# Kernel tuning notes

Measured on AMD Instinct MI355X. Metric: run time of the kernel, lower is better.

The kernel has to match this reference:

```python
import jax, jax.numpy as jnp
import numpy as np

D = 2048          # n_embd
F = 1408          # moe_inter_dim
E = 8             # n_routed_experts
TOPK = 2          # n_activated_experts
N_SHARED = 2
ROUTE_SCALE = 1.0


def setup_inputs() -> dict:
    key = jax.random.key(0)
    ks = jax.random.split(key, 8)
    s = 0.02
    x = jax.random.normal(ks[0], (2, 1024, D), dtype=jnp.float32)
    gate_w = jax.random.normal(ks[1], (D, E), dtype=jnp.float32) * s
    Fs = F * N_SHARED
    sw1 = jax.random.normal(ks[2], (D, Fs), dtype=jnp.float32) * s
    sw2 = jax.random.normal(ks[3], (Fs, D), dtype=jnp.float32) * s
    sw3 = jax.random.normal(ks[4], (D, Fs), dtype=jnp.float32) * s
    rw1 = jax.random.normal(ks[5], (E, D, F), dtype=jnp.float32) * s
    rw2 = jax.random.normal(ks[6], (E, F, D), dtype=jnp.float32) * s
    rw3 = jax.random.normal(ks[7], (E, D, F), dtype=jnp.float32) * s
    return {"x": x, "gate_w": gate_w, "sw1": sw1, "sw2": sw2, "sw3": sw3,
            "rw1": rw1, "rw2": rw2, "rw3": rw3}


def _swiglu(x, w1, w2, w3):
    return (jax.nn.silu(x @ w1) * (x @ w3)) @ w2


def reference(x, gate_w, sw1, sw2, sw3, rw1, rw2, rw3):
    B, T, _ = x.shape
    xf = x.reshape(-1, D)                       # [N, D]
    N = xf.shape[0]
    # shared experts (always applied)
    y = _swiglu(xf, sw1, sw2, sw3)              # [N, D]
    # gate: softmax scores, top-k (bias is None since n_embd != 7168; n_groups == 1)
    scores = jax.nn.softmax(xf @ gate_w, axis=-1)       # [N, E]
    weights, indices = jax.lax.top_k(scores, TOPK)       # gathered original scores
    weights = weights * ROUTE_SCALE
    # combine weights per (token, expert); zero for unassigned -> same math as
    # the per-expert gather/scatter loop in the original module
    cw = jnp.zeros((N, E), dtype=xf.dtype).at[jnp.arange(N)[:, None], indices].add(weights)
    for e in range(E):  # fixed small structural loop over experts
        h = _swiglu(xf, rw1[e], rw2[e], rw3[e])  # [N, D]
        y = y + cw[:, e:e + 1] * h
    return y.reshape(B, T, D)
```

## Files before the change

### kernel.cpp

```cpp
#include <hip/hip_runtime.h>
#include <hip/hip_bf16.h>
#include <math.h>

#define D_DIM 2048
#define F_DIM 1408
#define FS_DIM 2816
#define E_NUM 8
#define N_TOK 2048

typedef __attribute__((ext_vector_type(8))) short bf16x8;
typedef __attribute__((ext_vector_type(4))) float f32x4;

__device__ inline short f2bf(float f) {
    __hip_bfloat16 h = __float2bfloat16(f);
    return *reinterpret_cast<short*>(&h);
}
__device__ inline float bf2f(short s) {
    __hip_bfloat16 h; *reinterpret_cast<short*>(&h) = s;
    return __bfloat162float(h);
}
__device__ inline float silu1(float v) { return v / (1.f + expf(-v)); }

__device__ inline void async_copy16(const void* g, void* l) {
    __builtin_amdgcn_global_load_lds(
        (const __attribute__((address_space(1))) void*)g,
        (__attribute__((address_space(3))) void*)l, 16, 0, 0);
}

__device__ inline void t64(const float* in, short* out, int K, int N,
                           int kt, int nt, float (*tile)[65])
{
    int k0 = kt * 64, n0 = nt * 64;
    int t = threadIdx.x, tr = t >> 4, tc4 = (t & 15) * 4;
#pragma unroll
    for (int i = 0; i < 4; ++i) {
        int r = tr + i * 16;
        float4 v = *reinterpret_cast<const float4*>(in + (size_t)(k0 + r) * N + n0 + tc4);
        tile[r][tc4 + 0] = v.x; tile[r][tc4 + 1] = v.y;
        tile[r][tc4 + 2] = v.z; tile[r][tc4 + 3] = v.w;
    }
    __syncthreads();
#pragma unroll
    for (int i = 0; i < 4; ++i) {
        int n = tr + i * 16;
        short4 s4;
        s4.x = f2bf(tile[tc4 + 0][n]);
        s4.y = f2bf(tile[tc4 + 1][n]);
        s4.z = f2bf(tile[tc4 + 2][n]);
        s4.w = f2bf(tile[tc4 + 3][n]);
        *reinterpret_cast<short4*>(out + (size_t)(n0 + n) * K + k0 + tc4) = s4;
    }
}

__global__ __launch_bounds__(256) void prep_kernel(
    const float* __restrict__ x, const float* __restrict__ gw,
    float* __restrict__ assign_w, int* __restrict__ expert_count,
    int* __restrict__ expert_list, short* __restrict__ Xb,
    const float* __restrict__ sw1, short* __restrict__ swt1,
    const float* __restrict__ sw3, short* __restrict__ swt3,
    const float* __restrict__ rw1, short* __restrict__ rwt1,
    const float* __restrict__ rw3, short* __restrict__ rwt3)
{
    __shared__ float tile[64][65];
    int bid = blockIdx.x;
    int tid = threadIdx.x;
    if (bid < 512) {
        int wid = bid * 4 + (tid >> 6);
        int lane = tid & 63;
        const float* xr = x + (size_t)wid * D_DIM;
        float p[E_NUM];
#pragma unroll
        for (int e = 0; e < E_NUM; ++e) p[e] = 0.f;
        for (int d = lane; d < D_DIM; d += 64) {
            float xv = xr[d];
            const float4* g = reinterpret_cast<const float4*>(gw + (size_t)d * E_NUM);
            float4 g0 = g[0], g1 = g[1];
            p[0] = fmaf(xv, g0.x, p[0]); p[1] = fmaf(xv, g0.y, p[1]);
            p[2] = fmaf(xv, g0.z, p[2]); p[3] = fmaf(xv, g0.w, p[3]);
            p[4] = fmaf(xv, g1.x, p[4]); p[5] = fmaf(xv, g1.y, p[5]);
            p[6] = fmaf(xv, g1.z, p[6]); p[7] = fmaf(xv, g1.w, p[7]);
        }
#pragma unroll
        for (int off = 32; off > 0; off >>= 1)
#pragma unroll
            for (int e = 0; e < E_NUM; ++e)
                p[e] += __shfl_xor(p[e], off, 64);
        if (lane == 0) {
            float m = p[0];
#pragma unroll
            for (int e = 1; e < E_NUM; ++e) m = fmaxf(m, p[e]);
            float s = 0.f, pr[E_NUM];
#pragma unroll
            for (int e = 0; e < E_NUM; ++e) { pr[e] = expf(p[e] - m); s += pr[e]; }
            float inv = 1.f / s;
#pragma unroll
            for (int e = 0; e < E_NUM; ++e) pr[e] *= inv;
            int i0 = 0;
#pragma unroll
            for (int e = 1; e < E_NUM; ++e) if (pr[e] > pr[i0]) i0 = e;
            int i1 = (i0 == 0) ? 1 : 0;
#pragma unroll
            for (int e = 0; e < E_NUM; ++e) if (e != i0 && pr[e] > pr[i1]) i1 = e;
            int s0 = wid * 2, s1 = wid * 2 + 1;
            assign_w[s0] = pr[i0];
            assign_w[s1] = pr[i1];
            int p0 = atomicAdd(&expert_count[i0], 1);
            expert_list[i0 * N_TOK + p0] = s0;
            int p1 = atomicAdd(&expert_count[i1], 1);
            expert_list[i1 * N_TOK + p1] = s1;
        }
    } else if (bid < 2560) {
        int i = ((bid - 512) * 256 + tid) * 8;
        float4 v0 = *reinterpret_cast<const float4*>(x + i);
        float4 v1 = *reinterpret_cast<const float4*>(x + i + 4);
        bf16x8 o;
        o[0] = f2bf(v0.x); o[1] = f2bf(v0.y); o[2] = f2bf(v0.z); o[3] = f2bf(v0.w);
        o[4] = f2bf(v1.x); o[5] = f2bf(v1.y); o[6] = f2bf(v1.z); o[7] = f2bf(v1.w);
        *reinterpret_cast<bf16x8*>(Xb + i) = o;
    } else if (bid < 3968) {
        int t = bid - 2560;
        t64(sw1, swt1, D_DIM, FS_DIM, t % 32, t / 32, tile);
    } else if (bid < 5376) {
        int t = bid - 3968;
        t64(sw3, swt3, D_DIM, FS_DIM, t % 32, t / 32, tile);
    } else if (bid < 11008) {
        int t = bid - 5376;
        int e = t / 704, r = t % 704;
        t64(rw1 + (size_t)e * D_DIM * F_DIM, rwt1 + (size_t)e * F_DIM * D_DIM,
            D_DIM, F_DIM, r % 32, r / 32, tile);
    } else {
        int t = bid - 11008;
        int e = t / 704, r = t % 704;
        t64(rw3 + (size_t)e * D_DIM * F_DIM, rwt3 + (size_t)e * F_DIM * D_DIM,
            D_DIM, F_DIM, r % 32, r / 32, tile);
    }
}

__global__ __launch_bounds__(256) void moe_in_kernel(
    const short* __restrict__ Xb,
    const short* __restrict__ swt1, const short* __restrict__ swt3, short* __restrict__ Hs,
    const short* __restrict__ rwt1, const short* __restrict__ rwt3, short* __restrict__ Hr,
    const int* __restrict__ expert_list, const int* __restrict__ expert_count,
    const float* __restrict__ sw2, short* __restrict__ swt2,
    const float* __restrict__ rw2, short* __restrict__ rwt2)
{
    __shared__ char SMEM[32768];
    __shared__ int sl[128];
    int bid = blockIdx.x;
    int tid = threadIdx.x;

    if (bid >= 3584) {
        int t = bid - 3584;
        float (*tile)[65] = reinterpret_cast<float (*)[65]>(SMEM);
        if (t < 1408) {
            t64(sw2, swt2, FS_DIM, D_DIM, t % 44, t / 44, tile);
        } else {
            t -= 1408;
            int e = t / 704, r = t % 704;
            t64(rw2 + (size_t)e * F_DIM * D_DIM, rwt2 + (size_t)e * D_DIM * F_DIM,
                F_DIM, D_DIM, r % 22, r / 22, tile);
        }
        return;
    }

    int xcd = bid & 7, qq = bid >> 3, mtile = qq & 15, gq = qq >> 4;
    int g = gq * 8 + xcd;
    if (g >= 220) return;
    const short *W1, *W3;
    short* H;
    int ldH, n0, count;
    bool gather;
    const int* list = nullptr;
    int m0 = mtile * 128;
    if (g < 44) {
        gather = false; count = N_TOK;
        W1 = swt1; W3 = swt3; H = Hs; ldH = FS_DIM; n0 = g * 64;
    } else {
        int g2 = g - 44, e = g2 / 22;
        n0 = (g2 % 22) * 64;
        gather = true;
        count = expert_count[e];
        if (m0 >= count) return;
        list = expert_list + e * N_TOK;
        W1 = rwt1 + (size_t)e * F_DIM * D_DIM;
        W3 = rwt3 + (size_t)e * F_DIM * D_DIM;
        H = Hr; ldH = F_DIM;
    }
    if (tid < 128) {
        int rr = m0 + tid;
        sl[tid] = gather ? ((rr < count) ? list[rr] : -1) : rr;
    }
    __syncthreads();

    int l = tid & 63, w = tid >> 6;
    char* As  = SMEM;
    char* B1s = SMEM + 16384;
    char* B3s = SMEM + 24576;

    const char* aS[4];
#pragma unroll
    for (int j = 0; j < 4; ++j) {
        int r = (w * 4 + j) * 8 + (l >> 3);
        int s = sl[r];
        int tok = gather ? (s >= 0 ? (s >> 1) : 0) : s;
        aS[j] = (const char*)Xb + (size_t)tok * 4096 + (((l & 7) ^ (r & 7)) << 4);
    }
    const char* b1S[2]; const char* b3S[2];
#pragma unroll
    for (int j = 0; j < 2; ++j) {
        int r = (w * 2 + j) * 8 + (l >> 3);
        size_t off = (size_t)(n0 + r) * 4096 + (((l & 7) ^ (r & 7)) << 4);
        b1S[j] = (const char*)W1 + off;
        b3S[j] = (const char*)W3 + off;
    }

    int wm = w >> 1, wn = w & 1, frow = l & 15, fkg = l >> 4;
    f32x4 acc1[4][2], acc3[4][2];
#pragma unroll
    for (int i = 0; i < 4; ++i)
#pragma unroll
        for (int j = 0; j < 2; ++j) { acc1[i][j] = (f32x4)0.f; acc3[i][j] = (f32x4)0.f; }

    for (int it = 0; it < 32; ++it) {
        int kb = it << 7;
#pragma unroll
        for (int j = 0; j < 4; ++j)
            async_copy16(aS[j] + kb, As + (w * 4 + j) * 1024);
#pragma unroll
        for (int j = 0; j < 2; ++j) {
            async_copy16(b1S[j] + kb, B1s + (w * 2 + j) * 1024);
            async_copy16(b3S[j] + kb, B3s + (w * 2 + j) * 1024);
        }
        __syncthreads();
#pragma unroll
        for (int kk = 0; kk < 2; ++kk) {
            bf16x8 af[4], b1f[2], b3f[2];
#pragma unroll
            for (int mf = 0; mf < 4; ++mf) {
                int r = wm * 64 + mf * 16 + frow;
                af[mf] = *reinterpret_cast<const bf16x8*>(
                    As + r * 128 + ((((kk << 2) | fkg) ^ (r & 7)) << 4));
            }
#pragma unroll
            for (int nf = 0; nf < 2; ++nf) {
                int r = wn * 32 + nf * 16 + frow;
                int so = (((kk << 2) | fkg) ^ (r & 7)) << 4;
                b1f[nf] = *reinterpret_cast<const bf16x8*>(B1s + r * 128 + so);
                b3f[nf] = *reinterpret_cast<const bf16x8*>(B3s + r * 128 + so);
            }
#pragma unroll
            for (int mf = 0; mf < 4; ++mf)
#pragma unroll
                for (int nf = 0; nf < 2; ++nf) {
                    acc1[mf][nf] = __builtin_amdgcn_mfma_f32_16x16x32_bf16(
                        af[mf], b1f[nf], acc1[mf][nf], 0, 0, 0);
                    acc3[mf][nf] = __builtin_amdgcn_mfma_f32_16x16x32_bf16(
                        af[mf], b3f[nf], acc3[mf][nf], 0, 0, 0);
                }
        }
        __syncthreads();
    }

#pragma unroll
    for (int mf = 0; mf < 4; ++mf) {
#pragma unroll
        for (int jj = 0; jj < 4; ++jj) {
            int rl = wm * 64 + mf * 16 + fkg * 4 + jj;
            int s = sl[rl];
            if (s < 0) continue;
            short* hp = H + (size_t)s * ldH + n0 + wn * 32 + frow;
#pragma unroll
            for (int nf = 0; nf < 2; ++nf)
                hp[nf * 16] = f2bf(silu1(acc1[mf][nf][jj]) * acc3[mf][nf][jj]);
        }
    }
}

__global__ __launch_bounds__(256) void moe_out_kernel(
    const short* __restrict__ Hs, const short* __restrict__ swt2, float* __restrict__ Y,
    const short* __restrict__ Hr, const short* __restrict__ rwt2, short* __restrict__ H2,
    const int* __restrict__ expert_list, const int* __restrict__ expert_count)
{
    __shared__ char SMEM[24576];
    __shared__ int sl[128];
    int bid = blockIdx.x, tid = threadIdx.x;
    int xcd = bid & 7, qq = bid >> 3, mtile = qq & 15, gq = qq >> 4;
    int g = gq * 8 + xcd;
    if (g >= 288) return;
    const short *A, *B;
    int ldAb, NIT, n0, count;
    bool gather;
    const int* list = nullptr;
    int m0 = mtile * 128;
    if (g < 32) {
        gather = false; count = N_TOK;
        A = Hs; ldAb = FS_DIM * 2; NIT = 44; B = swt2; n0 = g * 64;
    } else {
        int g2 = g - 32, e = g2 >> 5;
        n0 = (g2 & 31) * 64;
        gather = true;
        count = expert_count[e];
        if (m0 >= count) return;
        list = expert_list + e * N_TOK;
        A = Hr; ldAb = F_DIM * 2; NIT = 22;
        B = rwt2 + (size_t)e * D_DIM * F_DIM;
    }
    if (tid < 128) {
        int rr = m0 + tid;
        sl[tid] = gather ? ((rr < count) ? list[rr] : -1) : rr;
    }
    __syncthreads();

    int l = tid & 63, w = tid >> 6;
    char* As = SMEM;
    char* Bs = SMEM + 16384;

    const char* aS[4];
#pragma unroll
    for (int j = 0; j < 4; ++j) {
        int r = (w * 4 + j) * 8 + (l >> 3);
        int s = sl[r];
        int arow = gather ? (s >= 0 ? s : 0) : s;
        aS[j] = (const char*)A + (size_t)arow * ldAb + (((l & 7) ^ (r & 7)) << 4);
    }
    const char* bS[2];
#pragma unroll
    for (int j = 0; j < 2; ++j) {
        int r = (w * 2 + j) * 8 + (l >> 3);
        bS[j] = (const char*)B + (size_t)(n0 + r) * ldAb + (((l & 7) ^ (r & 7)) << 4);
    }

    int wm = w >> 1, wn = w & 1, frow = l & 15, fkg = l >> 4;
    f32x4 acc[4][2];
#pragma unroll
    for (int i = 0; i < 4; ++i)
#pragma unroll
        for (int j = 0; j < 2; ++j) acc[i][j] = (f32x4)0.f;

    for (int it = 0; it < NIT; ++it) {
        int kb = it << 7;
#pragma unroll
        for (int j = 0; j < 4; ++j)
            async_copy16(aS[j] + kb, As + (w * 4 + j) * 1024);
#pragma unroll
        for (int j = 0; j < 2; ++j)
            async_copy16(bS[j] + kb, Bs + (w * 2 + j) * 1024);
        __syncthreads();
#pragma unroll
        for (int kk = 0; kk < 2; ++kk) {
            bf16x8 af[4], bf[2];
#pragma unroll
            for (int mf = 0; mf < 4; ++mf) {
                int r = wm * 64 + mf * 16 + frow;
                af[mf] = *reinterpret_cast<const bf16x8*>(
                    As + r * 128 + ((((kk << 2) | fkg) ^ (r & 7)) << 4));
            }
#pragma unroll
            for (int nf = 0; nf < 2; ++nf) {
                int r = wn * 32 + nf * 16 + frow;
                bf[nf] = *reinterpret_cast<const bf16x8*>(
                    Bs + r * 128 + ((((kk << 2) | fkg) ^ (r & 7)) << 4));
            }
#pragma unroll
            for (int mf = 0; mf < 4; ++mf)
#pragma unroll
                for (int nf = 0; nf < 2; ++nf)
                    acc[mf][nf] = __builtin_amdgcn_mfma_f32_16x16x32_bf16(
                        af[mf], bf[nf], acc[mf][nf], 0, 0, 0);
        }
        __syncthreads();
    }

#pragma unroll
    for (int mf = 0; mf < 4; ++mf) {
#pragma unroll
        for (int jj = 0; jj < 4; ++jj) {
            int rl = wm * 64 + mf * 16 + fkg * 4 + jj;
            int s = sl[rl];
            if (s < 0) continue;
            int col = n0 + wn * 32 + frow;
            if (!gather) {
                float* op = Y + (size_t)s * D_DIM + col;
#pragma unroll
                for (int nf = 0; nf < 2; ++nf)
                    op[nf * 16] = acc[mf][nf][jj];
            } else {
                short* op = H2 + (size_t)s * D_DIM + col;
#pragma unroll
                for (int nf = 0; nf < 2; ++nf)
                    op[nf * 16] = f2bf(acc[mf][nf][jj]);
            }
        }
    }
}

__global__ __launch_bounds__(256) void combine_kernel(
    float* __restrict__ Y, const short* __restrict__ H2,
    const float* __restrict__ assign_w)
{
    int tok = blockIdx.x, tid = threadIdx.x;
    float w0 = assign_w[2 * tok];
    float w1 = assign_w[2 * tok + 1];
    const short* h0 = H2 + (size_t)(2 * tok) * D_DIM + tid * 8;
    const short* h1 = h0 + D_DIM;
    bf16x8 a = *reinterpret_cast<const bf16x8*>(h0);
    bf16x8 b = *reinterpret_cast<const bf16x8*>(h1);
    float* y = Y + (size_t)tok * D_DIM + tid * 8;
    float4 y0 = *reinterpret_cast<float4*>(y);
    float4 y1 = *reinterpret_cast<float4*>(y + 4);
    y0.x = fmaf(w0, bf2f(a[0]), fmaf(w1, bf2f(b[0]), y0.x));
    y0.y = fmaf(w0, bf2f(a[1]), fmaf(w1, bf2f(b[1]), y0.y));
    y0.z = fmaf(w0, bf2f(a[2]), fmaf(w1, bf2f(b[2]), y0.z));
    y0.w = fmaf(w0, bf2f(a[3]), fmaf(w1, bf2f(b[3]), y0.w));
    y1.x = fmaf(w0, bf2f(a[4]), fmaf(w1, bf2f(b[4]), y1.x));
    y1.y = fmaf(w0, bf2f(a[5]), fmaf(w1, bf2f(b[5]), y1.y));
    y1.z = fmaf(w0, bf2f(a[6]), fmaf(w1, bf2f(b[6]), y1.z));
    y1.w = fmaf(w0, bf2f(a[7]), fmaf(w1, bf2f(b[7]), y1.w));
    *reinterpret_cast<float4*>(y) = y0;
    *reinterpret_cast<float4*>(y + 4) = y1;
}

extern "C" void kernel_launch(void* const* d_in, const int* in_sizes, int n_in,
                              void* d_out, int out_size, void* d_ws, size_t ws_size,
                              hipStream_t stream) {
    const float* x   = (const float*)d_in[0];
    const float* gw  = (const float*)d_in[1];
    const float* sw1 = (const float*)d_in[2];
    const float* sw2 = (const float*)d_in[3];
    const float* sw3 = (const float*)d_in[4];
    const float* rw1 = (const float*)d_in[5];
    const float* rw2 = (const float*)d_in[6];
    const float* rw3 = (const float*)d_in[7];
    float* Y = (float*)d_out;

    char* ws = (char*)d_ws;
    float* assign_w     = (float*)(ws);
    int*   expert_count = (int*)(ws + 16384);
    int*   expert_list  = (int*)(ws + 16384 + 256);

    const size_t XB_OFF   = 131072;
    const size_t SWT1_OFF = XB_OFF + 8388608ull;
    const size_t SWT3_OFF = SWT1_OFF + 11534336ull;
    const size_t SWT2_OFF = SWT3_OFF + 11534336ull;
    const size_t RWT1_OFF = SWT2_OFF + 11534336ull;
    const size_t RWT3_OFF = RWT1_OFF + 46137344ull;
    const size_t RWT2_OFF = RWT3_OFF + 46137344ull;
    const size_t HS_OFF   = RWT2_OFF + 46137344ull;
    const size_t HR_OFF   = HS_OFF + 11534336ull;
    const size_t H2_OFF   = HR_OFF + 11534336ull;

    short* Xb   = (short*)(ws + XB_OFF);
    short* swt1 = (short*)(ws + SWT1_OFF);
    short* swt3 = (short*)(ws + SWT3_OFF);
    short* swt2 = (short*)(ws + SWT2_OFF);
    short* rwt1 = (short*)(ws + RWT1_OFF);
    short* rwt3 = (short*)(ws + RWT3_OFF);
    short* rwt2 = (short*)(ws + RWT2_OFF);
    short* Hs   = (short*)(ws + HS_OFF);
    short* Hr   = (short*)(ws + HR_OFF);
    short* H2   = (short*)(ws + H2_OFF);

    hipMemsetAsync(expert_count, 0, E_NUM * sizeof(int), stream);

    prep_kernel<<<16640, 256, 0, stream>>>(
        x, gw, assign_w, expert_count, expert_list, Xb,
        sw1, swt1, sw3, swt3, rw1, rwt1, rw3, rwt3);

    moe_in_kernel<<<10624, 256, 0, stream>>>(
        Xb, swt1, swt3, Hs, rwt1, rwt3, Hr,
        expert_list, expert_count, sw2, swt2, rw2, rwt2);

    moe_out_kernel<<<4608, 256, 0, stream>>>(
        Hs, swt2, Y, Hr, rwt2, H2, expert_list, expert_count);

    combine_kernel<<<N_TOK, 256, 0, stream>>>(Y, H2, assign_w);
}
```

Measured before the change: 358.3 us.

## Enlarge GEMM tiles to 256x128 with 512 threads and double-buffered async loads

The MoE input and output GEMM kernels now use 512-thread blocks computing 256x128 tiles instead of 128x64. Each block double-buffers its LDS stages, issuing the next k-slice's global-to-LDS copies before computing on the current one and waiting with explicit vmcnt. This is meant to raise data reuse per block and hide load latency. In exchange it uses 96-128KB of LDS per block, which limits occupancy. Gathered-row indices are now read from global memory rather than staged in shared memory, and the weight-transpose blocks now process two tiles per block.

```diff
diff --git a/kernel.cpp b/kernel.cpp
--- a/kernel.cpp
+++ b/kernel.cpp
@@ -11,6 +11,8 @@
 typedef __attribute__((ext_vector_type(8))) short bf16x8;
 typedef __attribute__((ext_vector_type(4))) float f32x4;
 
+#define WAITVM(n) asm volatile("s_waitcnt vmcnt(" #n ")" ::: "memory")
+
 __device__ inline short f2bf(float f) {
     __hip_bfloat16 h = __float2bfloat16(f);
     return *reinterpret_cast<short*>(&h);
@@ -27,11 +29,11 @@
         (__attribute__((address_space(3))) void*)l, 16, 0, 0);
 }
 
-__device__ inline void t64(const float* in, short* out, int K, int N,
-                           int kt, int nt, float (*tile)[65])
+__device__ inline void t64h(const float* in, short* out, int K, int N,
+                            int kt, int nt, float (*tile)[65], int t)
 {
     int k0 = kt * 64, n0 = nt * 64;
-    int t = threadIdx.x, tr = t >> 4, tc4 = (t & 15) * 4;
+    int tr = t >> 4, tc4 = (t & 15) * 4;
 #pragma unroll
     for (int i = 0; i < 4; ++i) {
         int r = tr + i * 16;
@@ -119,24 +121,24 @@
         *reinterpret_cast<bf16x8*>(Xb + i) = o;
     } else if (bid < 3968) {
         int t = bid - 2560;
-        t64(sw1, swt1, D_DIM, FS_DIM, t % 32, t / 32, tile);
+        t64h(sw1, swt1, D_DIM, FS_DIM, t % 32, t / 32, tile, tid);
     } else if (bid < 5376) {
         int t = bid - 3968;
-        t64(sw3, swt3, D_DIM, FS_DIM, t % 32, t / 32, tile);
+        t64h(sw3, swt3, D_DIM, FS_DIM, t % 32, t / 32, tile, tid);
     } else if (bid < 11008) {
         int t = bid - 5376;
         int e = t / 704, r = t % 704;
-        t64(rw1 + (size_t)e * D_DIM * F_DIM, rwt1 + (size_t)e * F_DIM * D_DIM,
-            D_DIM, F_DIM, r % 32, r / 32, tile);
+        t64h(rw1 + (size_t)e * D_DIM * F_DIM, rwt1 + (size_t)e * F_DIM * D_DIM,
+             D_DIM, F_DIM, r % 32, r / 32, tile, tid);
     } else {
         int t = bid - 11008;
         int e = t / 704, r = t % 704;
-        t64(rw3 + (size_t)e * D_DIM * F_DIM, rwt3 + (size_t)e * F_DIM * D_DIM,
-            D_DIM, F_DIM, r % 32, r / 32, tile);
-    }
-}
-
-__global__ __launch_bounds__(256) void moe_in_kernel(
+        t64h(rw3 + (size_t)e * D_DIM * F_DIM, rwt3 + (size_t)e * F_DIM * D_DIM,
+             D_DIM, F_DIM, r % 32, r / 32, tile, tid);
+    }
+}
+
+__global__ __launch_bounds__(512) void moe_in_kernel(
     const short* __restrict__ Xb,
     const short* __restrict__ swt1, const short* __restrict__ swt3, short* __restrict__ Hs,
     const short* __restrict__ rwt1, const short* __restrict__ rwt3, short* __restrict__ Hr,
@@ -144,40 +146,39 @@
     const float* __restrict__ sw2, short* __restrict__ swt2,
     const float* __restrict__ rw2, short* __restrict__ rwt2)
 {
-    __shared__ char SMEM[32768];
-    __shared__ int sl[128];
-    int bid = blockIdx.x;
-    int tid = threadIdx.x;
-
-    if (bid >= 3584) {
-        int t = bid - 3584;
-        float (*tile)[65] = reinterpret_cast<float (*)[65]>(SMEM);
-        if (t < 1408) {
-            t64(sw2, swt2, FS_DIM, D_DIM, t % 44, t / 44, tile);
+    __shared__ char SMEM[131072];
+    int bid = blockIdx.x, tid = threadIdx.x;
+
+    if (bid >= 896) {
+        int t2 = (bid - 896) * 2 + (tid >> 8);
+        int t256 = tid & 255;
+        float (*tile)[65] = reinterpret_cast<float (*)[65]>(SMEM + (tid >> 8) * 16640);
+        if (t2 < 1408) {
+            t64h(sw2, swt2, FS_DIM, D_DIM, t2 % 44, t2 / 44, tile, t256);
         } else {
-            t -= 1408;
-            int e = t / 704, r = t % 704;
-            t64(rw2 + (size_t)e * F_DIM * D_DIM, rwt2 + (size_t)e * D_DIM * F_DIM,
-                F_DIM, D_DIM, r % 22, r / 22, tile);
+            int r = t2 - 1408;
+            int e = r / 704, rr = r % 704;
+            t64h(rw2 + (size_t)e * F_DIM * D_DIM, rwt2 + (size_t)e * D_DIM * F_DIM,
+                 F_DIM, D_DIM, rr % 22, rr / 22, tile, t256);
         }
         return;
     }
 
-    int xcd = bid & 7, qq = bid >> 3, mtile = qq & 15, gq = qq >> 4;
+    int xcd = bid & 7, qq = bid >> 3, mtile = qq & 7, gq = qq >> 3;
     int g = gq * 8 + xcd;
-    if (g >= 220) return;
+    if (g >= 110) return;
+    bool gather;
     const short *W1, *W3;
     short* H;
     int ldH, n0, count;
-    bool gather;
     const int* list = nullptr;
-    int m0 = mtile * 128;
-    if (g < 44) {
+    int m0 = mtile * 256;
+    if (g < 22) {
         gather = false; count = N_TOK;
-        W1 = swt1; W3 = swt3; H = Hs; ldH = FS_DIM; n0 = g * 64;
+        W1 = swt1; W3 = swt3; H = Hs; ldH = FS_DIM; n0 = g * 128;
     } else {
-        int g2 = g - 44, e = g2 / 22;
-        n0 = (g2 % 22) * 64;
+        int g2 = g - 22, e = g2 / 11;
+        n0 = (g2 % 11) * 128;
         gather = true;
         count = expert_count[e];
         if (m0 >= count) return;
@@ -186,79 +187,80 @@
         W3 = rwt3 + (size_t)e * F_DIM * D_DIM;
         H = Hr; ldH = F_DIM;
     }
-    if (tid < 128) {
-        int rr = m0 + tid;
-        sl[tid] = gather ? ((rr < count) ? list[rr] : -1) : rr;
-    }
-    __syncthreads();
 
     int l = tid & 63, w = tid >> 6;
-    char* As  = SMEM;
-    char* B1s = SMEM + 16384;
-    char* B3s = SMEM + 24576;
 
     const char* aS[4];
 #pragma unroll
     for (int j = 0; j < 4; ++j) {
-        int r = (w * 4 + j) * 8 + (l >> 3);
-        int s = sl[r];
-        int tok = gather ? (s >= 0 ? (s >> 1) : 0) : s;
-        aS[j] = (const char*)Xb + (size_t)tok * 4096 + (((l & 7) ^ (r & 7)) << 4);
-    }
-    const char* b1S[2]; const char* b3S[2];
+        int u = j * 512 + tid, r = u >> 3, s = u & 7;
+        int rr = m0 + r;
+        int tok = gather ? ((rr < count) ? (list[rr] >> 1) : 0) : rr;
+        aS[j] = (const char*)Xb + (size_t)tok * 4096 + ((s ^ (r & 7)) << 4);
+    }
+    const char *b1S[2], *b3S[2];
 #pragma unroll
     for (int j = 0; j < 2; ++j) {
-        int r = (w * 2 + j) * 8 + (l >> 3);
-        size_t off = (size_t)(n0 + r) * 4096 + (((l & 7) ^ (r & 7)) << 4);
+        int u = j * 512 + tid, r = u >> 3, s = u & 7;
+        size_t off = (size_t)(n0 + r) * 4096 + ((s ^ (r & 7)) << 4);
         b1S[j] = (const char*)W1 + off;
         b3S[j] = (const char*)W3 + off;
     }
 
+    auto STAGE = [&](int buf, int kb) {
+        char* base = SMEM + buf * 65536;
+#pragma unroll
+        for (int j = 0; j < 4; ++j)
+            async_copy16(aS[j] + kb, base + (j * 512 + tid) * 16);
+#pragma unroll
+        for (int j = 0; j < 2; ++j) {
+            async_copy16(b1S[j] + kb, base + 32768 + (j * 512 + tid) * 16);
+            async_copy16(b3S[j] + kb, base + 49152 + (j * 512 + tid) * 16);
+        }
+    };
+
     int wm = w >> 1, wn = w & 1, frow = l & 15, fkg = l >> 4;
-    f32x4 acc1[4][2], acc3[4][2];
+    f32x4 acc1[4][4], acc3[4][4];
 #pragma unroll
     for (int i = 0; i < 4; ++i)
 #pragma unroll
-        for (int j = 0; j < 2; ++j) { acc1[i][j] = (f32x4)0.f; acc3[i][j] = (f32x4)0.f; }
-
+        for (int j = 0; j < 4; ++j) { acc1[i][j] = (f32x4)0.f; acc3[i][j] = (f32x4)0.f; }
+
+    STAGE(0, 0);
+    int buf = 0;
     for (int it = 0; it < 32; ++it) {
-        int kb = it << 7;
-#pragma unroll
-        for (int j = 0; j < 4; ++j)
-            async_copy16(aS[j] + kb, As + (w * 4 + j) * 1024);
-#pragma unroll
-        for (int j = 0; j < 2; ++j) {
-            async_copy16(b1S[j] + kb, B1s + (w * 2 + j) * 1024);
-            async_copy16(b3S[j] + kb, B3s + (w * 2 + j) * 1024);
-        }
-        __syncthreads();
+        if (it < 31) { STAGE(buf ^ 1, (it + 1) << 7); WAITVM(8); }
+        else         { WAITVM(0); }
+        __builtin_amdgcn_s_barrier();
+        const char* base = SMEM + buf * 65536;
 #pragma unroll
         for (int kk = 0; kk < 2; ++kk) {
-            bf16x8 af[4], b1f[2], b3f[2];
+            bf16x8 af[4], b1f[4], b3f[4];
 #pragma unroll
             for (int mf = 0; mf < 4; ++mf) {
                 int r = wm * 64 + mf * 16 + frow;
                 af[mf] = *reinterpret_cast<const bf16x8*>(
-                    As + r * 128 + ((((kk << 2) | fkg) ^ (r & 7)) << 4));
+                    base + r * 128 + ((((kk << 2) | fkg) ^ (r & 7)) << 4));
             }
 #pragma unroll
-            for (int nf = 0; nf < 2; ++nf) {
-                int r = wn * 32 + nf * 16 + frow;
+            for (int nf = 0; nf < 4; ++nf) {
+                int r = wn * 64 + nf * 16 + frow;
                 int so = (((kk << 2) | fkg) ^ (r & 7)) << 4;
-                b1f[nf] = *reinterpret_cast<const bf16x8*>(B1s + r * 128 + so);
-                b3f[nf] = *reinterpret_cast<const bf16x8*>(B3s + r * 128 + so);
+                b1f[nf] = *reinterpret_cast<const bf16x8*>(base + 32768 + r * 128 + so);
+                b3f[nf] = *reinterpret_cast<const bf16x8*>(base + 49152 + r * 128 + so);
             }
 #pragma unroll
             for (int mf = 0; mf < 4; ++mf)
 #pragma unroll
-                for (int nf = 0; nf < 2; ++nf) {
+                for (int nf = 0; nf < 4; ++nf) {
                     acc1[mf][nf] = __builtin_amdgcn_mfma_f32_16x16x32_bf16(
                         af[mf], b1f[nf], acc1[mf][nf], 0, 0, 0);
                     acc3[mf][nf] = __builtin_amdgcn_mfma_f32_16x16x32_bf16(
                         af[mf], b3f[nf], acc3[mf][nf], 0, 0, 0);
                 }
         }
-        __syncthreads();
+        __builtin_amdgcn_s_barrier();
+        buf ^= 1;
     }
 
 #pragma unroll
@@ -266,109 +268,112 @@
 #pragma unroll
         for (int jj = 0; jj < 4; ++jj) {
             int rl = wm * 64 + mf * 16 + fkg * 4 + jj;
-            int s = sl[rl];
-            if (s < 0) continue;
-            short* hp = H + (size_t)s * ldH + n0 + wn * 32 + frow;
-#pragma unroll
-            for (int nf = 0; nf < 2; ++nf)
+            int rr = m0 + rl;
+            int s;
+            if (gather) { if (rr >= count) continue; s = list[rr]; }
+            else s = rr;
+            short* hp = H + (size_t)s * ldH + n0 + wn * 64 + frow;
+#pragma unroll
+            for (int nf = 0; nf < 4; ++nf)
                 hp[nf * 16] = f2bf(silu1(acc1[mf][nf][jj]) * acc3[mf][nf][jj]);
         }
     }
 }
 
-__global__ __launch_bounds__(256) void moe_out_kernel(
+__global__ __launch_bounds__(512) void moe_out_kernel(
     const short* __restrict__ Hs, const short* __restrict__ swt2, float* __restrict__ Y,
     const short* __restrict__ Hr, const short* __restrict__ rwt2, short* __restrict__ H2,
     const int* __restrict__ expert_list, const int* __restrict__ expert_count)
 {
-    __shared__ char SMEM[24576];
-    __shared__ int sl[128];
+    __shared__ char SMEM[98304];
     int bid = blockIdx.x, tid = threadIdx.x;
-    int xcd = bid & 7, qq = bid >> 3, mtile = qq & 15, gq = qq >> 4;
+    int xcd = bid & 7, qq = bid >> 3, mtile = qq & 7, gq = qq >> 3;
     int g = gq * 8 + xcd;
-    if (g >= 288) return;
+    if (g >= 144) return;
+    bool gather;
     const short *A, *B;
-    int ldAb, NIT, n0, count;
-    bool gather;
+    int ldKb, NIT, n0, count;
     const int* list = nullptr;
-    int m0 = mtile * 128;
-    if (g < 32) {
+    int m0 = mtile * 256;
+    if (g < 16) {
         gather = false; count = N_TOK;
-        A = Hs; ldAb = FS_DIM * 2; NIT = 44; B = swt2; n0 = g * 64;
+        A = Hs; ldKb = FS_DIM * 2; NIT = 44; B = swt2; n0 = g * 128;
     } else {
-        int g2 = g - 32, e = g2 >> 5;
-        n0 = (g2 & 31) * 64;
+        int g2 = g - 16, e = g2 >> 4;
+        n0 = (g2 & 15) * 128;
         gather = true;
         count = expert_count[e];
         if (m0 >= count) return;
         list = expert_list + e * N_TOK;
-        A = Hr; ldAb = F_DIM * 2; NIT = 22;
+        A = Hr; ldKb = F_DIM * 2; NIT = 22;
         B = rwt2 + (size_t)e * D_DIM * F_DIM;
     }
-    if (tid < 128) {
-        int rr = m0 + tid;
-        sl[tid] = gather ? ((rr < count) ? list[rr] : -1) : rr;
-    }
-    __syncthreads();
 
     int l = tid & 63, w = tid >> 6;
-    char* As = SMEM;
-    char* Bs = SMEM + 16384;
 
     const char* aS[4];
 #pragma unroll
     for (int j = 0; j < 4; ++j) {
-        int r = (w * 4 + j) * 8 + (l >> 3);
-        int s = sl[r];
-        int arow = gather ? (s >= 0 ? s : 0) : s;
-        aS[j] = (const char*)A + (size_t)arow * ldAb + (((l & 7) ^ (r & 7)) << 4);
+        int u = j * 512 + tid, r = u >> 3, s = u & 7;
+        int rr = m0 + r;
+        int arow = gather ? ((rr < count) ? list[rr] : 0) : rr;
+        aS[j] = (const char*)A + (size_t)arow * ldKb + ((s ^ (r & 7)) << 4);
     }
     const char* bS[2];
 #pragma unroll
     for (int j = 0; j < 2; ++j) {
-        int r = (w * 2 + j) * 8 + (l >> 3);
-        bS[j] = (const char*)B + (size_t)(n0 + r) * ldAb + (((l & 7) ^ (r & 7)) << 4);
-    }
+        int u = j * 512 + tid, r = u >> 3, s = u & 7;
+        bS[j] = (const char*)B + (size_t)(n0 + r) * ldKb + ((s ^ (r & 7)) << 4);
+    }
+
+    auto STAGE = [&](int buf, int kb) {
+        char* base = SMEM + buf * 49152;
+#pragma unroll
+        for (int j = 0; j < 4; ++j)
+            async_copy16(aS[j] + kb, base + (j * 512 + tid) * 16);
+#pragma unroll
+        for (int j = 0; j < 2; ++j)
+            async_copy16(bS[j] + kb, base + 32768 + (j * 512 + tid) * 16);
+    };
 
     int wm = w >> 1, wn = w & 1, frow = l & 15, fkg = l >> 4;
-    f32x4 acc[4][2];
+    f32x4 acc[4][4];
 #pragma unroll
     for (int i = 0; i < 4; ++i)
 #pragma unroll
-        for (int j = 0; j < 2; ++j) acc[i][j] = (f32x4)0.f;
-
+        for (int j = 0; j < 4; ++j) acc[i][j] = (f32x4)0.f;
+
+    STAGE(0, 0);
+    int buf = 0;
     for (int it = 0; it < NIT; ++it) {
-        int kb = it << 7;
-#pragma unroll
-        for (int j = 0; j < 4; ++j)
-            async_copy16(aS[j] + kb, As + (w * 4 + j) * 1024);
-#pragma unroll
-        for (int j = 0; j < 2; ++j)
-            async_copy16(bS[j] + kb, Bs + (w * 2 + j) * 1024);
-        __syncthreads();
+        if (it + 1 < NIT) { STAGE(buf ^ 1, (it + 1) << 7); WAITVM(6); }
+        else              { WAITVM(0); }
+        __builtin_amdgcn_s_barrier();
+        const char* base = SMEM + buf * 49152;
 #pragma unroll
         for (int kk = 0; kk < 2; ++kk) {
-            bf16x8 af[4], bf[2];
+            bf16x8 af[4], bf[4];
 #pragma unroll
             for (int mf = 0; mf < 4; ++mf) {
                 int r = wm * 64 + mf * 16 + frow;
                 af[mf] = *reinterpret_cast<const bf16x8*>(
-                    As + r * 128 + ((((kk << 2) | fkg) ^ (r & 7)) << 4));
+                    base + r * 128 + ((((kk << 2) | fkg) ^ (r & 7)) << 4));
             }
 #pragma unroll
-            for (int nf = 0; nf < 2; ++nf) {
-                int r = wn * 32 + nf * 16 + frow;
+            for (int nf = 0; nf < 4; ++nf) {
+                int r = wn * 64 + nf * 16 + frow;
                 bf[nf] = *reinterpret_cast<const bf16x8*>(
-                    Bs + r * 128 + ((((kk << 2) | fkg) ^ (r & 7)) << 4));
+                    base + 32768 + r * 128 + ((((kk << 2) | fkg) ^ (r & 7)) << 4));
             }
 #pragma unroll
             for (int mf = 0; mf < 4; ++mf)
 #pragma unroll
-                for (int nf = 0; nf < 2; ++nf)
+                for (int nf = 0; nf < 4; ++nf)
                     acc[mf][nf] = __builtin_amdgcn_mfma_f32_16x16x32_bf16(
                         af[mf], bf[nf], acc[mf][nf], 0, 0, 0);
         }
-        __syncthreads();
+        __builtin_amdgcn_s_barrier();
+        buf ^= 1;
     }
 
 #pragma unroll
@@ -376,18 +381,20 @@
 #pragma unroll
         for (int jj = 0; jj < 4; ++jj) {
             int rl = wm * 64 + mf * 16 + fkg * 4 + jj;
-            int s = sl[rl];
-            if (s < 0) continue;
-            int col = n0 + wn * 32 + frow;
+            int rr = m0 + rl;
+            int s;
+            if (gather) { if (rr >= count) continue; s = list[rr]; }
+            else s = rr;
+            int col = n0 + wn * 64 + frow;
             if (!gather) {
                 float* op = Y + (size_t)s * D_DIM + col;
 #pragma unroll
-                for (int nf = 0; nf < 2; ++nf)
+                for (int nf = 0; nf < 4; ++nf)
                     op[nf * 16] = acc[mf][nf][jj];
             } else {
                 short* op = H2 + (size_t)s * D_DIM + col;
 #pragma unroll
-                for (int nf = 0; nf < 2; ++nf)
+                for (int nf = 0; nf < 4; ++nf)
                     op[nf * 16] = f2bf(acc[mf][nf][jj]);
             }
         }
@@ -466,11 +473,11 @@
         x, gw, assign_w, expert_count, expert_list, Xb,
         sw1, swt1, sw3, swt3, rw1, rwt1, rw3, rwt3);
 
-    moe_in_kernel<<<10624, 256, 0, stream>>>(
+    moe_in_kernel<<<4416, 512, 0, stream>>>(
         Xb, swt1, swt3, Hs, rwt1, rwt3, Hr,
         expert_list, expert_count, sw2, swt2, rw2, rwt2);
 
-    moe_out_kernel<<<4608, 256, 0, stream>>>(
+    moe_out_kernel<<<1152, 512, 0, stream>>>(
         Hs, swt2, Y, Hr, rwt2, H2, expert_list, expert_count);
 
     combine_kernel<<<N_TOK, 256, 0, stream>>>(Y, H2, assign_w);
```

New measurement: 391.3 us. 1.09x slower.
